# Kernel optimization log

Hardware: AMD Instinct MI355X
Metric: run time of the kernel (lower is better)

## Reference

```python
import jax, jax.numpy as jnp
import numpy as np
from jax import lax

B, T, EMB = 16384, 50, 16
NS, ND, V = 8, 8, 100000
NEXP = 4
DNN_DIM = ND + NS * EMB + EMB + EMB + EMB  # 184
NEG_INF = float(-2**32 + 1)


def setup_inputs() -> dict:
    key = jax.random.key(0)
    ks = iter(jax.random.split(key, 40))
    def p(shape, s=0.05):
        return jax.random.normal(next(ks), shape, dtype=jnp.float32) * s
    inp = {
        'dense_inputs': jax.random.normal(next(ks), (B, ND), dtype=jnp.float32),
        'sparse_tables': p((NS, V, EMB)),
        'seq_table': p((V, EMB)),
        # DIN attention MLP: input dim 4*EMB = 64
        'att_w1': p((4 * EMB, 64)), 'att_b1': jnp.zeros((64,), jnp.float32),
        'att_w2': p((64, 32)),      'att_b2': jnp.zeros((32,), jnp.float32),
        'att_w3': p((32, 1)),       'att_b3': jnp.zeros((1,), jnp.float32),
        # GRU (reset_after=True, keras default): W [EMB,3H], U [H,3H], b [2,3H]
        'gru_W': p((EMB, 3 * EMB)), 'gru_U': p((EMB, 3 * EMB)),
        'gru_b': jnp.zeros((2, 3 * EMB), jnp.float32),
        # MMOE experts (stacked over expert axis)
        'ew1': p((NEXP, DNN_DIM, 128)), 'eb1': jnp.zeros((NEXP, 128), jnp.float32),
        'ew2': p((NEXP, 128, 64)),      'eb2': jnp.zeros((NEXP, 64), jnp.float32),
        'gfw': p((DNN_DIM, NEXP)), 'gfb': jnp.zeros((NEXP,), jnp.float32),
        'glw': p((DNN_DIM, NEXP)), 'glb': jnp.zeros((NEXP,), jnp.float32),
        'fw': p((64, 1)), 'fb': jnp.zeros((1,), jnp.float32),
        'lw': p((64, 1)), 'lb': jnp.zeros((1,), jnp.float32),
        'sparse_inputs': jax.random.randint(next(ks), (B, NS), 0, V, dtype=jnp.int32),
        'seq_input': jax.random.randint(next(ks), (B, T), 0, V, dtype=jnp.int32),
        'hist_input': jax.random.randint(next(ks), (B, T), 0, V, dtype=jnp.int32),
    }
    return inp


def _din_attention(query, keys, mask, w1, b1, w2, b2, w3, b3):
    # query [B,E], keys [B,T,E], mask [B,T] float (1 valid / 0 pad)
    q = jnp.broadcast_to(query[:, None, :], keys.shape)
    att_in = jnp.concatenate([q, keys, q - keys, q * keys], axis=-1)  # [B,T,4E]
    h = jax.nn.relu(att_in @ w1 + b1)
    h = jax.nn.relu(h @ w2 + b2)
    scores = (h @ w3 + b3)[..., 0]  # [B,T]
    scores = jnp.where(mask > 0, scores, NEG_INF)
    w = jax.nn.softmax(scores, axis=1)
    return jnp.sum(w[..., None] * keys, axis=1)  # [B,E]


def _gru(x, mask_bool, W, U, b):
    # x [B,T,E], mask_bool [B,T]; keras GRU reset_after=True, masked steps keep state
    b_i, b_r = b[0], b[1]
    x_all = x @ W + b_i  # [B,T,3H]
    def step(h, inp):
        x_t, m_t = inp  # [B,3H], [B]
        rec = h @ U + b_r
        xz, xr, xh = jnp.split(x_t, 3, axis=-1)
        rz, rr, rh = jnp.split(rec, 3, axis=-1)
        z = jax.nn.sigmoid(xz + rz)
        r = jax.nn.sigmoid(xr + rr)
        hh = jnp.tanh(xh + r * rh)
        h_new = z * h + (1.0 - z) * hh
        h = jnp.where(m_t[:, None], h_new, h)
        return h, None
    h0 = jnp.zeros((x.shape[0], U.shape[0]), x.dtype)
    h, _ = lax.scan(step, h0, (x_all.transpose(1, 0, 2), mask_bool.T))
    return h  # [B,H]


def reference(dense_inputs, sparse_tables, seq_table,
              att_w1, att_b1, att_w2, att_b2, att_w3, att_b3,
              gru_W, gru_U, gru_b,
              ew1, eb1, ew2, eb2, gfw, gfb, glw, glb, fw, fb, lw, lb,
              sparse_inputs, seq_input, hist_input):
    # sparse embeddings: [B, NS, E]
    sparse_embeds = jax.vmap(lambda t, idx: t[idx], in_axes=(0, 1), out_axes=1)(
        sparse_tables, sparse_inputs)
    sparse_flat = sparse_embeds.reshape(sparse_embeds.shape[0], -1)

    # seq feature: mean pool over time
    seq_flat = jnp.mean(seq_table[seq_input], axis=1)  # [B,E]

    # history: embeds via target item table (s0), DIN attention + GRU
    hist_emb = sparse_tables[0][hist_input]            # [B,T,E]
    mask_f = (hist_input != 0).astype(jnp.float32)
    target_emb = sparse_tables[0][sparse_inputs[:, 0]]  # [B,E]
    din_out = _din_attention(target_emb, hist_emb, mask_f,
                             att_w1, att_b1, att_w2, att_b2, att_w3, att_b3)
    gru_out = _gru(hist_emb, hist_input != 0, gru_W, gru_U, gru_b)

    dnn_input = jnp.concatenate(
        [dense_inputs, sparse_flat, seq_flat, din_out, gru_out], axis=-1)  # [B,184]

    # MMOE experts (dropout is identity at inference)
    h1 = jax.nn.relu(jnp.einsum('bd,edh->beh', dnn_input, ew1) + eb1)
    h2 = jax.nn.relu(jnp.einsum('beh,eho->beo', h1, ew2) + eb2)  # [B,NEXP,64]

    gate_f = jax.nn.softmax(dnn_input @ gfw + gfb, axis=-1)  # [B,NEXP]
    gate_l = jax.nn.softmax(dnn_input @ glw + glb, axis=-1)
    fin_in = jnp.einsum('be,beo->bo', gate_f, h2)
    lik_in = jnp.einsum('be,beo->bo', gate_l, h2)

    finish = jax.nn.sigmoid(fin_in @ fw + fb)  # [B,1]
    like = jax.nn.sigmoid(lik_in @ lw + lb)    # [B,1]
    return finish, like
```

## Files before the change

kernel.cpp:

```cpp
#include <hip/hip_runtime.h>

#define BB 16384
#define TT 50
#define EMBD 16
#define NSP 8
#define NDD 8
#define VV 100000
#define DNN 184
#define NEGINF (-4294967295.0f)

__device__ __forceinline__ float sigmoidf_(float x) { return 1.0f / (1.0f + __expf(-x)); }
__device__ __forceinline__ float tanhf_(float x) { return 1.0f - 2.0f / (__expf(2.0f * x) + 1.0f); }

__global__ __launch_bounds__(256, 5) void k1_fused(
    const float* __restrict__ dense,
    const float* __restrict__ tables,
    const float* __restrict__ seq_table,
    const float* __restrict__ aw1, const float* __restrict__ ab1,
    const float* __restrict__ aw2, const float* __restrict__ ab2,
    const float* __restrict__ aw3, const float* __restrict__ ab3,
    const float* __restrict__ gW, const float* __restrict__ gU, const float* __restrict__ gB,
    const int* __restrict__ sparse_in, const int* __restrict__ seq_in, const int* __restrict__ hist_in,
    float* __restrict__ dnn_out)
{
    const int w = threadIdx.x >> 6;
    const int lane = threadIdx.x & 63;
    const int b = blockIdx.x * 4 + w;

    __shared__ float histE[4][64][16];
    __shared__ float maskL[4][64];
    __shared__ float qsh[4][16];
    __shared__ float dnnL[4][DNN];
    __shared__ float wsoft[4][64];

    if (lane < TT) {
        int hidx = hist_in[b * TT + lane];
        const float4* src = (const float4*)(tables + (size_t)hidx * EMBD);
        float4 a0 = src[0], a1 = src[1], a2 = src[2], a3 = src[3];
        *(float4*)&histE[w][lane][0]  = a0;
        *(float4*)&histE[w][lane][4]  = a1;
        *(float4*)&histE[w][lane][8]  = a2;
        *(float4*)&histE[w][lane][12] = a3;
        maskL[w][lane] = (hidx != 0) ? 1.0f : 0.0f;
    } else {
        float4 z = make_float4(0.f, 0.f, 0.f, 0.f);
        *(float4*)&histE[w][lane][0]  = z;
        *(float4*)&histE[w][lane][4]  = z;
        *(float4*)&histE[w][lane][8]  = z;
        *(float4*)&histE[w][lane][12] = z;
        maskL[w][lane] = 0.0f;
    }
    if (lane < EMBD) {
        int ti = sparse_in[b * NSP];
        qsh[w][lane] = tables[(size_t)ti * EMBD + lane];
    }
    if (lane < NDD) dnnL[w][lane] = dense[b * NDD + lane];
    for (int i = lane; i < NSP * EMBD; i += 64) {
        int s = i >> 4, j = i & 15;
        int idx = sparse_in[b * NSP + s];
        dnnL[w][NDD + i] = tables[((size_t)s * VV + idx) * EMBD + j];
    }
    {
        int g = lane >> 4, j = lane & 15;
        float acc = 0.0f;
        for (int t = g; t < TT; t += 4) {
            int idx = seq_in[b * TT + t];
            acc += seq_table[(size_t)idx * EMBD + j];
        }
        acc += __shfl_xor(acc, 16);
        acc += __shfl_xor(acc, 32);
        if (lane < EMBD) dnnL[w][NDD + NSP * EMBD + lane] = acc * (1.0f / TT);
    }
    __syncthreads();

    float q[EMBD], k[EMBD];
    {
        float4 q0 = *(const float4*)&qsh[w][0],  q1 = *(const float4*)&qsh[w][4];
        float4 q2 = *(const float4*)&qsh[w][8],  q3 = *(const float4*)&qsh[w][12];
        q[0]=q0.x; q[1]=q0.y; q[2]=q0.z; q[3]=q0.w; q[4]=q1.x; q[5]=q1.y; q[6]=q1.z; q[7]=q1.w;
        q[8]=q2.x; q[9]=q2.y; q[10]=q2.z; q[11]=q2.w; q[12]=q3.x; q[13]=q3.y; q[14]=q3.z; q[15]=q3.w;
        float4 k0 = *(const float4*)&histE[w][lane][0],  k1 = *(const float4*)&histE[w][lane][4];
        float4 k2 = *(const float4*)&histE[w][lane][8],  k3 = *(const float4*)&histE[w][lane][12];
        k[0]=k0.x; k[1]=k0.y; k[2]=k0.z; k[3]=k0.w; k[4]=k1.x; k[5]=k1.y; k[6]=k1.z; k[7]=k1.w;
        k[8]=k2.x; k[9]=k2.y; k[10]=k2.z; k[11]=k2.w; k[12]=k3.x; k[13]=k3.y; k[14]=k3.z; k[15]=k3.w;
    }
    float mask = maskL[w][lane];

    float h2a[32];
    #pragma unroll
    for (int i = 0; i < 32; ++i) h2a[i] = ab2[i];

    for (int c = 0; c < 4; ++c) {
        float h1c[16];
        #pragma unroll
        for (int jj = 0; jj < 16; ++jj) h1c[jj] = ab1[c * 16 + jj];
        #pragma unroll 4
        for (int j = 0; j < 16; ++j) {
            float qa = q[j], ka = k[j];
            float qmk = qa - ka, qk = qa * ka;
            const float* r0 = aw1 + j * 64 + c * 16;
            const float* r1 = r0 + 16 * 64;
            const float* r2 = r0 + 32 * 64;
            const float* r3 = r0 + 48 * 64;
            #pragma unroll
            for (int jj = 0; jj < 16; ++jj)
                h1c[jj] += qa * r0[jj] + ka * r1[jj] + qmk * r2[jj] + qk * r3[jj];
        }
        #pragma unroll 4
        for (int jj = 0; jj < 16; ++jj) {
            float hv = fmaxf(h1c[jj], 0.0f);
            const float* w2r = aw2 + (c * 16 + jj) * 32;
            #pragma unroll
            for (int i = 0; i < 32; ++i) h2a[i] += hv * w2r[i];
        }
    }
    float score = ab3[0];
    #pragma unroll
    for (int i = 0; i < 32; ++i) score += fmaxf(h2a[i], 0.0f) * aw3[i];

    score = (lane < TT && mask > 0.0f) ? score : NEGINF;
    float m = score;
    #pragma unroll
    for (int off = 32; off > 0; off >>= 1) m = fmaxf(m, __shfl_xor(m, off));
    float e = (lane < TT) ? __expf(score - m) : 0.0f;
    float ssum = e;
    #pragma unroll
    for (int off = 32; off > 0; off >>= 1) ssum += __shfl_xor(ssum, off);
    wsoft[w][lane] = e / ssum;
    __syncthreads();
    if (lane < EMBD) {
        float acc = 0.0f;
        for (int t = 0; t < TT; ++t) acc += wsoft[w][t] * histE[w][t][lane];
        dnnL[w][NDD + NSP * EMBD + EMBD + lane] = acc;
    }

    float Wc[EMBD], Uc[EMBD], bi = 0.0f, br = 0.0f;
    if (lane < 48) {
        #pragma unroll
        for (int v = 0; v < EMBD; ++v) { Wc[v] = gW[v * 48 + lane]; Uc[v] = gU[v * 48 + lane]; }
        bi = gB[lane]; br = gB[48 + lane];
    }
    float hcur = 0.0f;
    for (int t = 0; t < TT; ++t) {
        float4 x0 = *(const float4*)&histE[w][t][0];
        float4 x1 = *(const float4*)&histE[w][t][4];
        float4 x2 = *(const float4*)&histE[w][t][8];
        float4 x3 = *(const float4*)&histE[w][t][12];
        float mt = maskL[w][t];
        float hv[16];
        #pragma unroll
        for (int v = 0; v < 16; ++v) hv[v] = __shfl(hcur, v);
        float xa = bi, rc = br;
        xa += x0.x*Wc[0] + x0.y*Wc[1] + x0.z*Wc[2] + x0.w*Wc[3];
        xa += x1.x*Wc[4] + x1.y*Wc[5] + x1.z*Wc[6] + x1.w*Wc[7];
        xa += x2.x*Wc[8] + x2.y*Wc[9] + x2.z*Wc[10] + x2.w*Wc[11];
        xa += x3.x*Wc[12] + x3.y*Wc[13] + x3.z*Wc[14] + x3.w*Wc[15];
        #pragma unroll
        for (int v = 0; v < 16; ++v) rc += hv[v] * Uc[v];
        float xr = __shfl(xa, lane + 16), xh = __shfl(xa, lane + 32);
        float rr = __shfl(rc, lane + 16), rh = __shfl(rc, lane + 32);
        float z  = sigmoidf_(xa + rc);
        float r  = sigmoidf_(xr + rr);
        float hh = tanhf_(xh + r * rh);
        float hnew = z * hcur + (1.0f - z) * hh;
        hcur = (mt > 0.0f) ? hnew : hcur;
    }
    if (lane < EMBD) dnnL[w][DNN - EMBD + lane] = hcur;
    __syncthreads();

    for (int i = lane; i < DNN; i += 64)
        dnn_out[(size_t)b * DNN + i] = dnnL[w][i];
}

#define BBT 8
__global__ __launch_bounds__(256) void k2_mmoe(
    const float* __restrict__ dnn_in,
    const float* __restrict__ ew1, const float* __restrict__ eb1,
    const float* __restrict__ ew2, const float* __restrict__ eb2,
    const float* __restrict__ gfw, const float* __restrict__ gfb,
    const float* __restrict__ glw, const float* __restrict__ glb,
    const float* __restrict__ fw, const float* __restrict__ fb,
    const float* __restrict__ lw, const float* __restrict__ lb,
    float* __restrict__ out)
{
    const int tid = threadIdx.x;
    const int b0 = blockIdx.x * BBT;

    __shared__ float dlds[BBT * DNN];
    __shared__ float h1L[BBT][512];
    __shared__ float h2L[BBT][256];
    __shared__ float gateL[BBT][8];

    {
        const float* drow = dnn_in + (size_t)b0 * DNN;
        for (int i = tid; i < BBT * DNN; i += 256) dlds[i] = drow[i];
    }
    __syncthreads();

    {
        int col0 = tid;
        int e0 = col0 >> 7, i0 = col0 & 127;
        const float* wp0 = ew1 + (size_t)e0 * DNN * 128 + i0;
        const float* wp1 = ew1 + (size_t)(e0 + 2) * DNN * 128 + i0;
        float acc0[BBT], acc1[BBT];
        float bias0 = eb1[col0], bias1 = eb1[col0 + 256];
        #pragma unroll
        for (int bb = 0; bb < BBT; ++bb) { acc0[bb] = bias0; acc1[bb] = bias1; }
        for (int d = 0; d < DNN; d += 4) {
            float w00 = wp0[(size_t)(d + 0) * 128], w01 = wp0[(size_t)(d + 1) * 128];
            float w02 = wp0[(size_t)(d + 2) * 128], w03 = wp0[(size_t)(d + 3) * 128];
            float w10 = wp1[(size_t)(d + 0) * 128], w11 = wp1[(size_t)(d + 1) * 128];
            float w12 = wp1[(size_t)(d + 2) * 128], w13 = wp1[(size_t)(d + 3) * 128];
            #pragma unroll
            for (int bb = 0; bb < BBT; ++bb) {
                const float4 h4 = *(const float4*)&dlds[bb * DNN + d];
                acc0[bb] += h4.x * w00 + h4.y * w01 + h4.z * w02 + h4.w * w03;
                acc1[bb] += h4.x * w10 + h4.y * w11 + h4.z * w12 + h4.w * w13;
            }
        }
        #pragma unroll
        for (int bb = 0; bb < BBT; ++bb) {
            h1L[bb][col0]       = fmaxf(acc0[bb], 0.0f);
            h1L[bb][col0 + 256] = fmaxf(acc1[bb], 0.0f);
        }
    }

    if (tid < 64) {
        int bb = tid >> 3, which = (tid >> 2) & 1, eidx = tid & 3;
        const float* gw = which ? glw : gfw;
        float acc = which ? glb[eidx] : gfb[eidx];
        for (int d = 0; d < DNN; ++d) acc += dlds[bb * DNN + d] * gw[d * 4 + eidx];
        gateL[bb][which * 4 + eidx] = acc;
    }
    __syncthreads();

    if (tid < 16) {
        int bb = tid >> 1, which = tid & 1;
        float l0 = gateL[bb][which * 4 + 0], l1 = gateL[bb][which * 4 + 1];
        float l2 = gateL[bb][which * 4 + 2], l3 = gateL[bb][which * 4 + 3];
        float mm = fmaxf(fmaxf(l0, l1), fmaxf(l2, l3));
        float e0 = __expf(l0 - mm), e1 = __expf(l1 - mm), e2 = __expf(l2 - mm), e3 = __expf(l3 - mm);
        float ss = e0 + e1 + e2 + e3;
        gateL[bb][which * 4 + 0] = e0 / ss; gateL[bb][which * 4 + 1] = e1 / ss;
        gateL[bb][which * 4 + 2] = e2 / ss; gateL[bb][which * 4 + 3] = e3 / ss;
    }

    {
        int col = tid;
        int eidx = col >> 6, i = col & 63;
        const float* wp = ew2 + (size_t)eidx * 128 * 64 + i;
        float acc[BBT];
        float bias = eb2[col];
        #pragma unroll
        for (int bb = 0; bb < BBT; ++bb) acc[bb] = bias;
        for (int d = 0; d < 128; d += 4) {
            float w0 = wp[(d + 0) * 64], w1v = wp[(d + 1) * 64];
            float w2v = wp[(d + 2) * 64], w3v = wp[(d + 3) * 64];
            #pragma unroll
            for (int bb = 0; bb < BBT; ++bb) {
                const float4 h4 = *(const float4*)&h1L[bb][eidx * 128 + d];
                acc[bb] += h4.x * w0 + h4.y * w1v + h4.z * w2v + h4.w * w3v;
            }
        }
        #pragma unroll
        for (int bb = 0; bb < BBT; ++bb) h2L[bb][col] = fmaxf(acc[bb], 0.0f);
    }
    __syncthreads();

    {
        int wv = tid >> 6, lane = tid & 63;
        for (int it = 0; it < 2; ++it) {
            int bb = wv * 2 + it;
            float h0 = h2L[bb][lane], h1v = h2L[bb][64 + lane];
            float h2v = h2L[bb][128 + lane], h3v = h2L[bb][192 + lane];
            float fin = gateL[bb][0] * h0 + gateL[bb][1] * h1v + gateL[bb][2] * h2v + gateL[bb][3] * h3v;
            float lik = gateL[bb][4] * h0 + gateL[bb][5] * h1v + gateL[bb][6] * h2v + gateL[bb][7] * h3v;
            float pf = fin * fw[lane];
            float pl = lik * lw[lane];
            #pragma unroll
            for (int off = 32; off > 0; off >>= 1) {
                pf += __shfl_xor(pf, off);
                pl += __shfl_xor(pl, off);
            }
            if (lane == 0) {
                out[b0 + bb]      = sigmoidf_(pf + fb[0]);
                out[BB + b0 + bb] = sigmoidf_(pl + lb[0]);
            }
        }
    }
}

extern "C" void kernel_launch(void* const* d_in, const int* in_sizes, int n_in,
                              void* d_out, int out_size, void* d_ws, size_t ws_size,
                              hipStream_t stream)
{
    const float* dense     = (const float*)d_in[0];
    const float* tables    = (const float*)d_in[1];
    const float* seq_table = (const float*)d_in[2];
    const float* aw1 = (const float*)d_in[3];  const float* ab1 = (const float*)d_in[4];
    const float* aw2 = (const float*)d_in[5];  const float* ab2 = (const float*)d_in[6];
    const float* aw3 = (const float*)d_in[7];  const float* ab3 = (const float*)d_in[8];
    const float* gW  = (const float*)d_in[9];  const float* gU  = (const float*)d_in[10];
    const float* gB  = (const float*)d_in[11];
    const float* ew1 = (const float*)d_in[12]; const float* eb1 = (const float*)d_in[13];
    const float* ew2 = (const float*)d_in[14]; const float* eb2 = (const float*)d_in[15];
    const float* gfw = (const float*)d_in[16]; const float* gfb = (const float*)d_in[17];
    const float* glw = (const float*)d_in[18]; const float* glb = (const float*)d_in[19];
    const float* fw  = (const float*)d_in[20]; const float* fb  = (const float*)d_in[21];
    const float* lw  = (const float*)d_in[22]; const float* lb  = (const float*)d_in[23];
    const int* sparse_in = (const int*)d_in[24];
    const int* seq_in    = (const int*)d_in[25];
    const int* hist_in   = (const int*)d_in[26];
    float* out = (float*)d_out;
    float* dnn_ws = (float*)d_ws;

    hipLaunchKernelGGL(k1_fused, dim3(BB / 4), dim3(256), 0, stream,
                       dense, tables, seq_table, aw1, ab1, aw2, ab2, aw3, ab3,
                       gW, gU, gB, sparse_in, seq_in, hist_in, dnn_ws);
    hipLaunchKernelGGL(k2_mmoe, dim3(BB / BBT), dim3(256), 0, stream,
                       dnn_ws, ew1, eb1, ew2, eb2, gfw, gfb, glw, glb,
                       fw, fb, lw, lb, out);
}
```

Before: 582.8 us.

## Compute DIN attention MLP with bf16 MFMA instead of scalar FMAs

Replaces the per-lane scalar fp32 attention MLP (64->64->32) with bf16 MFMA 16x16x32 tiles. Each wave packs its query/key features into an LDS bf16 tile, runs both layers on matrix cores, and reduces the final 32->1 projection with shuffles. The attention-weighted sum now uses all lanes, and blocks shrink to 2 waves. This cuts the large VALU FMA count of the attention MLP at the cost of bf16 precision in the scores, extra LDS traffic and reloading the weights into registers in every block.

```diff
diff --git a/kernel.cpp b/kernel.cpp
--- a/kernel.cpp
+++ b/kernel.cpp
@@ -9,10 +9,22 @@
 #define DNN 184
 #define NEGINF (-4294967295.0f)
 
+typedef float f32x4 __attribute__((ext_vector_type(4)));
+typedef short bf16x8 __attribute__((ext_vector_type(8)));
+
 __device__ __forceinline__ float sigmoidf_(float x) { return 1.0f / (1.0f + __expf(-x)); }
 __device__ __forceinline__ float tanhf_(float x) { return 1.0f - 2.0f / (__expf(2.0f * x) + 1.0f); }
 
-__global__ __launch_bounds__(256, 5) void k1_fused(
+__device__ __forceinline__ unsigned short f2bf(float x) {
+    union { float f; unsigned u; } c; c.f = x;
+    unsigned r = c.u + 0x7FFFu + ((c.u >> 16) & 1u);
+    return (unsigned short)(r >> 16);
+}
+__device__ __forceinline__ unsigned pack2(float lo, float hi) {
+    return (unsigned)f2bf(lo) | ((unsigned)f2bf(hi) << 16);
+}
+
+__global__ __launch_bounds__(128, 3) void k1_fused(
     const float* __restrict__ dense,
     const float* __restrict__ tables,
     const float* __restrict__ seq_table,
@@ -25,13 +37,15 @@
 {
     const int w = threadIdx.x >> 6;
     const int lane = threadIdx.x & 63;
-    const int b = blockIdx.x * 4 + w;
-
-    __shared__ float histE[4][64][16];
-    __shared__ float maskL[4][64];
-    __shared__ float qsh[4][16];
-    __shared__ float dnnL[4][DNN];
-    __shared__ float wsoft[4][64];
+    const int b = blockIdx.x * 2 + w;
+    const int g = lane >> 4, r16 = lane & 15;
+
+    __shared__ __align__(16) float histE[2][64][16];
+    __shared__ float maskL[2][64];
+    __shared__ float qsh[2][16];
+    __shared__ float dnnL[2][DNN];
+    __shared__ float wsoft[2][64];
+    __shared__ __align__(16) unsigned short attB[2][64][72];
 
     if (lane < TT) {
         int hidx = hist_in[b * TT + lane];
@@ -61,9 +75,9 @@
         dnnL[w][NDD + i] = tables[((size_t)s * VV + idx) * EMBD + j];
     }
     {
-        int g = lane >> 4, j = lane & 15;
+        int gg = lane >> 4, j = lane & 15;
         float acc = 0.0f;
-        for (int t = g; t < TT; t += 4) {
+        for (int t = gg; t < TT; t += 4) {
             int idx = seq_in[b * TT + t];
             acc += seq_table[(size_t)idx * EMBD + j];
         }
@@ -73,51 +87,103 @@
     }
     __syncthreads();
 
-    float q[EMBD], k[EMBD];
-    {
-        float4 q0 = *(const float4*)&qsh[w][0],  q1 = *(const float4*)&qsh[w][4];
-        float4 q2 = *(const float4*)&qsh[w][8],  q3 = *(const float4*)&qsh[w][12];
-        q[0]=q0.x; q[1]=q0.y; q[2]=q0.z; q[3]=q0.w; q[4]=q1.x; q[5]=q1.y; q[6]=q1.z; q[7]=q1.w;
-        q[8]=q2.x; q[9]=q2.y; q[10]=q2.z; q[11]=q2.w; q[12]=q3.x; q[13]=q3.y; q[14]=q3.z; q[15]=q3.w;
-        float4 k0 = *(const float4*)&histE[w][lane][0],  k1 = *(const float4*)&histE[w][lane][4];
-        float4 k2 = *(const float4*)&histE[w][lane][8],  k3 = *(const float4*)&histE[w][lane][12];
-        k[0]=k0.x; k[1]=k0.y; k[2]=k0.z; k[3]=k0.w; k[4]=k1.x; k[5]=k1.y; k[6]=k1.z; k[7]=k1.w;
-        k[8]=k2.x; k[9]=k2.y; k[10]=k2.z; k[11]=k2.w; k[12]=k3.x; k[13]=k3.y; k[14]=k3.z; k[15]=k3.w;
-    }
+    bf16x8 a1f[4][2];
+    #pragma unroll
+    for (int mt = 0; mt < 4; ++mt)
+        #pragma unroll
+        for (int kc = 0; kc < 2; ++kc)
+            #pragma unroll
+            for (int j = 0; j < 8; ++j)
+                a1f[mt][kc][j] = (short)f2bf(aw1[(kc * 32 + g * 8 + j) * 64 + mt * 16 + r16]);
+    bf16x8 a2f[2][2];
+    #pragma unroll
+    for (int mt = 0; mt < 2; ++mt)
+        #pragma unroll
+        for (int kc = 0; kc < 2; ++kc)
+            #pragma unroll
+            for (int j = 0; j < 8; ++j)
+                a2f[mt][kc][j] = (short)f2bf(aw2[(kc * 32 + g * 8 + j) * 32 + mt * 16 + r16]);
+
+    {
+        float qv[16], kv[16];
+        #pragma unroll
+        for (int j = 0; j < 16; ++j) { qv[j] = qsh[w][j]; kv[j] = histE[w][lane][j]; }
+        unsigned short* rowp = &attB[w][lane][0];
+        uint4 u;
+        u.x = pack2(qv[0], qv[1]);   u.y = pack2(qv[2], qv[3]);
+        u.z = pack2(qv[4], qv[5]);   u.w = pack2(qv[6], qv[7]);
+        *(uint4*)&rowp[0] = u;
+        u.x = pack2(qv[8], qv[9]);   u.y = pack2(qv[10], qv[11]);
+        u.z = pack2(qv[12], qv[13]); u.w = pack2(qv[14], qv[15]);
+        *(uint4*)&rowp[8] = u;
+        u.x = pack2(kv[0], kv[1]);   u.y = pack2(kv[2], kv[3]);
+        u.z = pack2(kv[4], kv[5]);   u.w = pack2(kv[6], kv[7]);
+        *(uint4*)&rowp[16] = u;
+        u.x = pack2(kv[8], kv[9]);   u.y = pack2(kv[10], kv[11]);
+        u.z = pack2(kv[12], kv[13]); u.w = pack2(kv[14], kv[15]);
+        *(uint4*)&rowp[24] = u;
+        u.x = pack2(qv[0]-kv[0], qv[1]-kv[1]);   u.y = pack2(qv[2]-kv[2], qv[3]-kv[3]);
+        u.z = pack2(qv[4]-kv[4], qv[5]-kv[5]);   u.w = pack2(qv[6]-kv[6], qv[7]-kv[7]);
+        *(uint4*)&rowp[32] = u;
+        u.x = pack2(qv[8]-kv[8], qv[9]-kv[9]);   u.y = pack2(qv[10]-kv[10], qv[11]-kv[11]);
+        u.z = pack2(qv[12]-kv[12], qv[13]-kv[13]); u.w = pack2(qv[14]-kv[14], qv[15]-kv[15]);
+        *(uint4*)&rowp[40] = u;
+        u.x = pack2(qv[0]*kv[0], qv[1]*kv[1]);   u.y = pack2(qv[2]*kv[2], qv[3]*kv[3]);
+        u.z = pack2(qv[4]*kv[4], qv[5]*kv[5]);   u.w = pack2(qv[6]*kv[6], qv[7]*kv[7]);
+        *(uint4*)&rowp[48] = u;
+        u.x = pack2(qv[8]*kv[8], qv[9]*kv[9]);   u.y = pack2(qv[10]*kv[10], qv[11]*kv[11]);
+        u.z = pack2(qv[12]*kv[12], qv[13]*kv[13]); u.w = pack2(qv[14]*kv[14], qv[15]*kv[15]);
+        *(uint4*)&rowp[56] = u;
+    }
+    __syncthreads();
+
+    #pragma unroll
+    for (int nt = 0; nt < 4; ++nt) {
+        const unsigned short* rp = &attB[w][nt * 16 + r16][g * 8];
+        bf16x8 b0 = *(const bf16x8*)(rp);
+        bf16x8 b1 = *(const bf16x8*)(rp + 32);
+        #pragma unroll
+        for (int mt = 0; mt < 4; ++mt) {
+            f32x4 acc = {0.f, 0.f, 0.f, 0.f};
+            acc = __builtin_amdgcn_mfma_f32_16x16x32_bf16(a1f[mt][0], b0, acc, 0, 0, 0);
+            acc = __builtin_amdgcn_mfma_f32_16x16x32_bf16(a1f[mt][1], b1, acc, 0, 0, 0);
+            const float4 bia = *(const float4*)(ab1 + mt * 16 + g * 4);
+            float v0 = fmaxf(acc[0] + bia.x, 0.0f);
+            float v1 = fmaxf(acc[1] + bia.y, 0.0f);
+            float v2 = fmaxf(acc[2] + bia.z, 0.0f);
+            float v3 = fmaxf(acc[3] + bia.w, 0.0f);
+            uint2 pw; pw.x = pack2(v0, v1); pw.y = pack2(v2, v3);
+            *(uint2*)&attB[w][nt * 16 + r16][mt * 16 + g * 4] = pw;
+        }
+    }
+
+    float snt[4];
+    #pragma unroll
+    for (int nt = 0; nt < 4; ++nt) {
+        const unsigned short* rp = &attB[w][nt * 16 + r16][g * 8];
+        bf16x8 c0 = *(const bf16x8*)(rp);
+        bf16x8 c1 = *(const bf16x8*)(rp + 32);
+        float sp = 0.0f;
+        #pragma unroll
+        for (int mt = 0; mt < 2; ++mt) {
+            f32x4 acc = {0.f, 0.f, 0.f, 0.f};
+            acc = __builtin_amdgcn_mfma_f32_16x16x32_bf16(a2f[mt][0], c0, acc, 0, 0, 0);
+            acc = __builtin_amdgcn_mfma_f32_16x16x32_bf16(a2f[mt][1], c1, acc, 0, 0, 0);
+            const float4 bia = *(const float4*)(ab2 + mt * 16 + g * 4);
+            const float4 w3v = *(const float4*)(aw3 + mt * 16 + g * 4);
+            sp += fmaxf(acc[0] + bia.x, 0.0f) * w3v.x;
+            sp += fmaxf(acc[1] + bia.y, 0.0f) * w3v.y;
+            sp += fmaxf(acc[2] + bia.z, 0.0f) * w3v.z;
+            sp += fmaxf(acc[3] + bia.w, 0.0f) * w3v.w;
+        }
+        sp += __shfl_xor(sp, 16);
+        sp += __shfl_xor(sp, 32);
+        snt[nt] = sp;
+    }
+    float score = (g == 0) ? snt[0] : (g == 1) ? snt[1] : (g == 2) ? snt[2] : snt[3];
+    score += ab3[0];
+
     float mask = maskL[w][lane];
-
-    float h2a[32];
-    #pragma unroll
-    for (int i = 0; i < 32; ++i) h2a[i] = ab2[i];
-
-    for (int c = 0; c < 4; ++c) {
-        float h1c[16];
-        #pragma unroll
-        for (int jj = 0; jj < 16; ++jj) h1c[jj] = ab1[c * 16 + jj];
-        #pragma unroll 4
-        for (int j = 0; j < 16; ++j) {
-            float qa = q[j], ka = k[j];
-            float qmk = qa - ka, qk = qa * ka;
-            const float* r0 = aw1 + j * 64 + c * 16;
-            const float* r1 = r0 + 16 * 64;
-            const float* r2 = r0 + 32 * 64;
-            const float* r3 = r0 + 48 * 64;
-            #pragma unroll
-            for (int jj = 0; jj < 16; ++jj)
-                h1c[jj] += qa * r0[jj] + ka * r1[jj] + qmk * r2[jj] + qk * r3[jj];
-        }
-        #pragma unroll 4
-        for (int jj = 0; jj < 16; ++jj) {
-            float hv = fmaxf(h1c[jj], 0.0f);
-            const float* w2r = aw2 + (c * 16 + jj) * 32;
-            #pragma unroll
-            for (int i = 0; i < 32; ++i) h2a[i] += hv * w2r[i];
-        }
-    }
-    float score = ab3[0];
-    #pragma unroll
-    for (int i = 0; i < 32; ++i) score += fmaxf(h2a[i], 0.0f) * aw3[i];
-
     score = (lane < TT && mask > 0.0f) ? score : NEGINF;
     float m = score;
     #pragma unroll
@@ -128,10 +194,13 @@
     for (int off = 32; off > 0; off >>= 1) ssum += __shfl_xor(ssum, off);
     wsoft[w][lane] = e / ssum;
     __syncthreads();
-    if (lane < EMBD) {
-        float acc = 0.0f;
-        for (int t = 0; t < TT; ++t) acc += wsoft[w][t] * histE[w][t][lane];
-        dnnL[w][NDD + NSP * EMBD + EMBD + lane] = acc;
+
+    {
+        float da = 0.0f;
+        for (int t = g; t < TT; t += 4) da += wsoft[w][t] * histE[w][t][r16];
+        da += __shfl_xor(da, 16);
+        da += __shfl_xor(da, 32);
+        if (lane < EMBD) dnnL[w][NDD + NSP * EMBD + EMBD + lane] = da;
     }
 
     float Wc[EMBD], Uc[EMBD], bi = 0.0f, br = 0.0f;
@@ -314,7 +383,7 @@
     float* out = (float*)d_out;
     float* dnn_ws = (float*)d_ws;
 
-    hipLaunchKernelGGL(k1_fused, dim3(BB / 4), dim3(256), 0, stream,
+    hipLaunchKernelGGL(k1_fused, dim3(BB / 2), dim3(128), 0, stream,
                        dense, tables, seq_table, aw1, ab1, aw2, ab2, aw3, ab3,
                        gW, gU, gB, sparse_in, seq_in, hist_in, dnn_ws);
     hipLaunchKernelGGL(k2_mmoe, dim3(BB / BBT), dim3(256), 0, stream,
```

New measurement: 528.5 us. -9.3%, faster.
